# Kernel optimization log

Hardware: AMD Instinct MI355X
Metric: run time of the kernel (lower is better)

The kernel has to match this reference:

```python
import jax, jax.numpy as jnp
import numpy as np

ALPHA = 0.2        # LeakyReLU negative slope (self.alpha)
NEG = -9e15        # mask value used by the torch module


def gru_cell(x, h, W_ih, W_hh, b_ih, b_hh):
    """torch.nn.GRUCell math. x, h: [N, F]; W_*: [3F, F]; b_*: [3F]. Gate order r,z,n."""
    gi = x @ W_ih.T + b_ih
    gh = h @ W_hh.T + b_hh
    ir, iz, i_n = jnp.split(gi, 3, axis=-1)
    hr, hz, h_n = jnp.split(gh, 3, axis=-1)
    r = jax.nn.sigmoid(ir + hr)
    z = jax.nn.sigmoid(iz + hz)
    n = jnp.tanh(i_n + r * h_n)
    return (1.0 - z) * n + z * h


def setup_inputs() -> dict:
    key = jax.random.key(0)
    N, F = 8192, 256
    ks = jax.random.split(key, 8)
    inputs = jax.random.normal(ks[0], (N, F), jnp.float32)
    # GRUCell parameters
    W_ih = jax.random.normal(ks[1], (3 * F, F), jnp.float32) / np.sqrt(F)
    W_hh = jax.random.normal(ks[2], (3 * F, F), jnp.float32) / np.sqrt(F)
    b_ih = jax.random.normal(ks[3], (3 * F,), jnp.float32) * 0.01
    b_hh = jax.random.normal(ks[4], (3 * F,), jnp.float32) * 0.01
    # GAT attention vector a: [2F, 1]
    a = jax.random.normal(ks[5], (2 * F, 1), jnp.float32) / np.sqrt(2.0 * F)
    # per-node neighbor pair (encodes weight_dict's 1-/2-neighbor cases)
    nbr = jax.random.randint(ks[6], (N, 2), 0, N)
    # dense adjacency, values in {0,1}
    adj = jax.random.randint(ks[7], (N, N), 0, 2).astype(jnp.int32)
    return dict(inputs=inputs, W_ih=W_ih, W_hh=W_hh, b_ih=b_ih, b_hh=b_hh,
                a=a, nbr=nbr, adj=adj)


def reference(inputs, W_ih, W_hh, b_ih, b_hh, a, nbr, adj):
    F_dim = inputs.shape[1]
    # per-node GRU aggregation: hidden = neighbor1 feature, input = neighbor2 feature
    h = inputs[nbr[:, 0]]                      # [N, F]
    x = inputs[nbr[:, 1]]                      # [N, F]
    outs = gru_cell(x, h, W_ih, W_hh, b_ih, b_hh)  # [N, F]
    # GAT scores: e[i,j] = leakyrelu([outs_i || outs_j] . a) = leakyrelu(f1_i + f2_j)
    # (decomposed -- avoids materializing the [N*N, 2F] concat of the original)
    a1 = a[:F_dim, 0]                          # [F]
    a2 = a[F_dim:, 0]                          # [F]
    e = jax.nn.leaky_relu((outs @ a1)[:, None] + (outs @ a2)[None, :], ALPHA)  # [N, N]
    e = jnp.where(adj > 0, e, NEG)
    return jax.nn.softmax(e, axis=1)
```

## Files before the change

### kernel.cpp

```cpp
#include <hip/hip_runtime.h>
#include <hip/hip_bf16.h>

#define NN 8192
#define FF 256
#define NEGV -9000000000000000.0f

typedef __bf16 bf16x8 __attribute__((ext_vector_type(8)));
typedef float f32x4 __attribute__((ext_vector_type(4)));
typedef int i32x4 __attribute__((ext_vector_type(4)));

__global__ __launch_bounds__(256) void k_pack(const float* __restrict__ Wih,
                                              const float* __restrict__ Whh,
                                              __hip_bfloat16* __restrict__ Wc) {
  const int o = blockIdx.x * 256 + threadIdx.x;
  const int l = o & 63;
  const int ks = (o >> 6) & 7;
  const int w = (o >> 9) & 3;
  const int fbb = (o >> 11) & 3;
  const int g = o >> 13;
  const int row = g * 256 + fbb * 64 + w * 16 + (l & 15);
  const int col = (l >> 4) * 8 + ks * 32;
  const float* src = (row < 768) ? (Wih + (size_t)row * FF + col)
                                 : (Whh + (size_t)(row - 768) * FF + col);
  const float4 v0 = *(const float4*)src;
  const float4 v1 = *(const float4*)(src + 4);
  union { __hip_bfloat16 h[8]; uint4 u; } t;
  t.h[0] = __float2bfloat16(v0.x); t.h[1] = __float2bfloat16(v0.y);
  t.h[2] = __float2bfloat16(v0.z); t.h[3] = __float2bfloat16(v0.w);
  t.h[4] = __float2bfloat16(v1.x); t.h[5] = __float2bfloat16(v1.y);
  t.h[6] = __float2bfloat16(v1.z); t.h[7] = __float2bfloat16(v1.w);
  *(uint4*)(Wc + (size_t)o * 8) = t.u;
}

__global__ __launch_bounds__(256) void k_gru(const __hip_bfloat16* __restrict__ Wpk,
                                             const float* __restrict__ inputs,
                                             const int* __restrict__ nbr,
                                             const float* __restrict__ b_ih,
                                             const float* __restrict__ b_hh,
                                             const float* __restrict__ a,
                                             float* __restrict__ p1a,
                                             float* __restrict__ p2a) {
  __shared__ __align__(16) __hip_bfloat16 Ax[16 * 256];
  __shared__ __align__(16) __hip_bfloat16 Ah[16 * 256];
  __shared__ int hrow_s[16];
  __shared__ float r1[4][16], r2[4][16];
  const int rb = blockIdx.x * 16;
  const int fb = blockIdx.y;
  const int tid = threadIdx.x;
  const int w = tid >> 6, l = tid & 63;
  const int fl = l & 15, q = l >> 4;

  if (tid < 16) hrow_s[tid] = nbr[2 * (rb + tid)];

#pragma unroll
  for (int j = 0; j < 2; ++j) {
    const int r = w * 4 + j * 2 + (l >> 5);
    const int gc = l & 31;
    const int xr = nbr[2 * (rb + r) + 1];
    const int hr_ = nbr[2 * (rb + r)];
    const float4 xv0 = *(const float4*)(inputs + (size_t)xr * FF + gc * 8);
    const float4 xv1 = *(const float4*)(inputs + (size_t)xr * FF + gc * 8 + 4);
    const float4 hv0 = *(const float4*)(inputs + (size_t)hr_ * FF + gc * 8);
    const float4 hv1 = *(const float4*)(inputs + (size_t)hr_ * FF + gc * 8 + 4);
    union { __hip_bfloat16 hh[8]; uint4 u; } tx, th;
    tx.hh[0] = __float2bfloat16(xv0.x); tx.hh[1] = __float2bfloat16(xv0.y);
    tx.hh[2] = __float2bfloat16(xv0.z); tx.hh[3] = __float2bfloat16(xv0.w);
    tx.hh[4] = __float2bfloat16(xv1.x); tx.hh[5] = __float2bfloat16(xv1.y);
    tx.hh[6] = __float2bfloat16(xv1.z); tx.hh[7] = __float2bfloat16(xv1.w);
    th.hh[0] = __float2bfloat16(hv0.x); th.hh[1] = __float2bfloat16(hv0.y);
    th.hh[2] = __float2bfloat16(hv0.z); th.hh[3] = __float2bfloat16(hv0.w);
    th.hh[4] = __float2bfloat16(hv1.x); th.hh[5] = __float2bfloat16(hv1.y);
    th.hh[6] = __float2bfloat16(hv1.z); th.hh[7] = __float2bfloat16(hv1.w);
    *(uint4*)((char*)Ax + r * 512 + (gc ^ (r & 7)) * 16) = tx.u;
    *(uint4*)((char*)Ah + r * 512 + (gc ^ (r & 7)) * 16) = th.u;
  }
  __syncthreads();

  const int f = fb * 64 + w * 16 + fl;
  const float bir = b_ih[f], biz = b_ih[256 + f], bin_ = b_ih[512 + f];
  const float bhr = b_hh[f], bhz = b_hh[256 + f], bhn = b_hh[512 + f];
  const float a1f = a[f], a2f = a[256 + f];

  f32x4 acc[6];
#pragma unroll
  for (int g = 0; g < 6; ++g) acc[g] = (f32x4){0, 0, 0, 0};

  bf16x8 axf[8], ahf[8];
#pragma unroll
  for (int ks = 0; ks < 8; ++ks) {
    const int c = ks * 4 + q;
    axf[ks] = *(const bf16x8*)((const char*)Ax + fl * 512 + (c ^ (fl & 7)) * 16);
    ahf[ks] = *(const bf16x8*)((const char*)Ah + fl * 512 + (c ^ (fl & 7)) * 16);
  }
#pragma unroll
  for (int g = 0; g < 3; ++g) {
    const int bi = ((g * 16 + fb * 4 + w) * 8) * 64 + l;
    const int bh = (((3 + g) * 16 + fb * 4 + w) * 8) * 64 + l;
#pragma unroll
    for (int ks = 0; ks < 8; ++ks) {
      const bf16x8 bfi = *(const bf16x8*)(Wpk + (size_t)(bi + ks * 64) * 8);
      const bf16x8 bfh = *(const bf16x8*)(Wpk + (size_t)(bh + ks * 64) * 8);
      acc[g]     = __builtin_amdgcn_mfma_f32_16x16x32_bf16(axf[ks], bfi, acc[g], 0, 0, 0);
      acc[3 + g] = __builtin_amdgcn_mfma_f32_16x16x32_bf16(ahf[ks], bfh, acc[3 + g], 0, 0, 0);
    }
  }

  float p1[4], p2[4];
#pragma unroll
  for (int j = 0; j < 4; ++j) {
    const int row = q * 4 + j;
    const float ir = acc[0][j] + bir;
    const float iz = acc[1][j] + biz;
    const float in_ = acc[2][j] + bin_;
    const float hrv = acc[3][j] + bhr;
    const float hzv = acc[4][j] + bhz;
    const float hnv = acc[5][j] + bhn;
    const float r_ = 1.f / (1.f + __expf(-(ir + hrv)));
    const float z_ = 1.f / (1.f + __expf(-(iz + hzv)));
    const float n_ = tanhf(in_ + r_ * hnv);
    const float hval = inputs[(size_t)hrow_s[row] * FF + f];
    const float o = (1.f - z_) * n_ + z_ * hval;
    p1[j] = o * a1f;
    p2[j] = o * a2f;
  }

#pragma unroll
  for (int j = 0; j < 4; ++j) {
#pragma unroll
    for (int off = 1; off < 16; off <<= 1) {
      p1[j] += __shfl_xor(p1[j], off);
      p2[j] += __shfl_xor(p2[j], off);
    }
  }
  if (fl == 0) {
#pragma unroll
    for (int j = 0; j < 4; ++j) {
      r1[w][q * 4 + j] = p1[j];
      r2[w][q * 4 + j] = p2[j];
    }
  }
  __syncthreads();
  if (tid < 16) {
    p1a[fb * NN + rb + tid] = r1[0][tid] + r1[1][tid] + r1[2][tid] + r1[3][tid];
  } else if (tid < 32) {
    const int t2 = tid - 16;
    p2a[fb * NN + rb + t2] = r2[0][t2] + r2[1][t2] + r2[2][t2] + r2[3][t2];
  }
}

__global__ __launch_bounds__(256) void k_reduce(const float* __restrict__ p1a,
                                                const float* __restrict__ p2a,
                                                float* __restrict__ s1,
                                                float* __restrict__ s2) {
  const int i = blockIdx.x * 256 + threadIdx.x;
  s1[i] = p1a[i] + p1a[NN + i] + p1a[2 * NN + i] + p1a[3 * NN + i];
  s2[i] = p2a[i] + p2a[NN + i] + p2a[2 * NN + i] + p2a[3 * NN + i];
}

__global__ __launch_bounds__(256, 5) void k_softmax(const int* __restrict__ adj,
                                                    const float* __restrict__ s1,
                                                    const float* __restrict__ s2,
                                                    float* __restrict__ out) {
  __shared__ float red[4];
  const int row = blockIdx.x;
  const int t = threadIdx.x;
  const i32x4* adjv = (const i32x4*)(adj + (size_t)row * NN);
  i32x4 a4[8];
#pragma unroll
  for (int k = 0; k < 8; ++k) a4[k] = __builtin_nontemporal_load(adjv + k * 256 + t);
  f32x4 sv[8];
#pragma unroll
  for (int k = 0; k < 8; ++k) sv[k] = *(const f32x4*)(s2 + (k * 256 + t) * 4);
  const float s1v = s1[row];

  float tsum = 0.f;
#pragma unroll
  for (int k = 0; k < 8; ++k) {
#pragma unroll
    for (int c = 0; c < 4; ++c) {
      float x = s1v + sv[k][c];
      x = (x > 0.f) ? x : 0.2f * x;
      x = (a4[k][c] > 0) ? x : NEGV;
      tsum += __expf(x);
    }
  }
#pragma unroll
  for (int off = 32; off; off >>= 1) tsum += __shfl_xor(tsum, off);
  if ((t & 63) == 0) red[t >> 6] = tsum;
  __syncthreads();
  const float inv = 1.f / (red[0] + red[1] + red[2] + red[3]);
  float* orow = out + (size_t)row * NN;
#pragma unroll
  for (int k = 0; k < 8; ++k) {
    const int v = k * 256 + t;
    f32x4 o;
#pragma unroll
    for (int c = 0; c < 4; ++c) {
      float x = s1v + sv[k][c];
      x = (x > 0.f) ? x : 0.2f * x;
      x = (a4[k][c] > 0) ? x : NEGV;
      o[c] = __expf(x) * inv;
    }
    __builtin_nontemporal_store(o, (f32x4*)(orow + v * 4));
  }
}

extern "C" void kernel_launch(void* const* d_in, const int* in_sizes, int n_in,
                              void* d_out, int out_size, void* d_ws, size_t ws_size,
                              hipStream_t stream) {
  const float* inputs = (const float*)d_in[0];
  const float* W_ih   = (const float*)d_in[1];
  const float* W_hh   = (const float*)d_in[2];
  const float* b_ih   = (const float*)d_in[3];
  const float* b_hh   = (const float*)d_in[4];
  const float* a      = (const float*)d_in[5];
  const int*   nbr    = (const int*)d_in[6];
  const int*   adj    = (const int*)d_in[7];
  float* out = (float*)d_out;

  __hip_bfloat16* Wpk = (__hip_bfloat16*)((char*)d_out + (80u << 20));
  float* p1a = (float*)((char*)d_out + (96u << 20));
  float* p2a = p1a + 4 * NN;
  float* s1 = (float*)d_ws;
  float* s2 = s1 + NN;

  k_pack<<<192, 256, 0, stream>>>(W_ih, W_hh, Wpk);
  k_gru<<<dim3(512, 4), 256, 0, stream>>>(Wpk, inputs, nbr, b_ih, b_hh, a, p1a, p2a);
  k_reduce<<<32, 256, 0, stream>>>(p1a, p2a, s1, s2);
  k_softmax<<<NN, 256, 0, stream>>>(adj, s1, s2, out);
}
```

Before: 121.6 us.

## Split masked softmax into bitmask-and-sum pass and output-write pass

Replaces the single fused softmax kernel with two kernels. The first reads the adjacency, packs it into a per-row bitmask and computes each row's inverse exp-sum. The second recomputes the scores from the bitmask and streams the normalized output. This aims to separate read-heavy and write-heavy phases and reduce register pressure so occupancy can rise. It costs an extra launch plus a small bitmask round trip, and falls back to the old kernel when the workspace is too small.

Measured after the change: 129.2 us. 6.2% more time.

```diff
diff --git a/kernel.cpp b/kernel.cpp
--- a/kernel.cpp
+++ b/kernel.cpp
@@ -157,6 +157,67 @@
   s2[i] = p2a[i] + p2a[NN + i] + p2a[2 * NN + i] + p2a[3 * NN + i];
 }
 
+__global__ __launch_bounds__(256, 8) void k_mask(const int* __restrict__ adj,
+                                                 const float* __restrict__ s1,
+                                                 const float* __restrict__ s2,
+                                                 unsigned* __restrict__ bits,
+                                                 float* __restrict__ invv) {
+  __shared__ float red[4];
+  const int row = blockIdx.x;
+  const int t = threadIdx.x;
+  const i32x4* adjv = (const i32x4*)(adj + (size_t)row * NN);
+  const float s1v = s1[row];
+
+  unsigned m = 0u;
+  float tsum = 0.f;
+#pragma unroll
+  for (int k = 0; k < 8; ++k) {
+    const i32x4 a4 = __builtin_nontemporal_load(adjv + k * 256 + t);
+    const f32x4 sv = *(const f32x4*)(s2 + (k * 256 + t) * 4);
+#pragma unroll
+    for (int c = 0; c < 4; ++c) {
+      float x = s1v + sv[c];
+      x = (x > 0.f) ? x : 0.2f * x;
+      const bool on = a4[c] > 0;
+      m |= (on ? 1u : 0u) << (k * 4 + c);
+      x = on ? x : NEGV;
+      tsum += __expf(x);
+    }
+  }
+  bits[(size_t)row * 256 + t] = m;
+#pragma unroll
+  for (int off = 32; off; off >>= 1) tsum += __shfl_xor(tsum, off);
+  if ((t & 63) == 0) red[t >> 6] = tsum;
+  __syncthreads();
+  if (t == 0) invv[row] = 1.f / (red[0] + red[1] + red[2] + red[3]);
+}
+
+__global__ __launch_bounds__(256, 8) void k_write(const unsigned* __restrict__ bits,
+                                                  const float* __restrict__ s1,
+                                                  const float* __restrict__ s2,
+                                                  const float* __restrict__ invv,
+                                                  float* __restrict__ out) {
+  const int row = blockIdx.x;
+  const int t = threadIdx.x;
+  const unsigned m = bits[(size_t)row * 256 + t];
+  const float s1v = s1[row];
+  const float inv = invv[row];
+  float* orow = out + (size_t)row * NN;
+#pragma unroll
+  for (int k = 0; k < 8; ++k) {
+    const f32x4 sv = *(const f32x4*)(s2 + (k * 256 + t) * 4);
+    f32x4 o;
+#pragma unroll
+    for (int c = 0; c < 4; ++c) {
+      float x = s1v + sv[c];
+      x = (x > 0.f) ? x : 0.2f * x;
+      x = ((m >> (k * 4 + c)) & 1u) ? x : NEGV;
+      o[c] = __expf(x) * inv;
+    }
+    __builtin_nontemporal_store(o, (f32x4*)(orow + (k * 256 + t) * 4));
+  }
+}
+
 __global__ __launch_bounds__(256, 5) void k_softmax(const int* __restrict__ adj,
                                                     const float* __restrict__ s1,
                                                     const float* __restrict__ s2,
@@ -223,9 +284,17 @@
   float* p2a = p1a + 4 * NN;
   float* s1 = (float*)d_ws;
   float* s2 = s1 + NN;
+  float* invv = s2 + NN;
+  unsigned* bits = (unsigned*)((char*)d_ws + 96 * 1024);
 
   k_pack<<<192, 256, 0, stream>>>(W_ih, W_hh, Wpk);
   k_gru<<<dim3(512, 4), 256, 0, stream>>>(Wpk, inputs, nbr, b_ih, b_hh, a, p1a, p2a);
   k_reduce<<<32, 256, 0, stream>>>(p1a, p2a, s1, s2);
-  k_softmax<<<NN, 256, 0, stream>>>(adj, s1, s2, out);
-}
+
+  if (ws_size >= (size_t)(9u << 20)) {
+    k_mask<<<NN, 256, 0, stream>>>(adj, s1, s2, bits, invv);
+    k_write<<<NN, 256, 0, stream>>>(bits, s1, s2, invv, out);
+  } else {
+    k_softmax<<<NN, 256, 0, stream>>>(adj, s1, s2, out);
+  }
+}
```
